# Kernel tuning notes

Hardware: AMD Instinct MI355X
Metric: run time of the kernel (lower is better)

The kernel has to match this reference:

```python
import jax, jax.numpy as jnp
import numpy as np


def setup_inputs() -> dict:
    key = jax.random.key(0)
    N, nH, D, L, P = 2, 8, 32, 4, 4
    shapes = np.array([[92, 92], [46, 46], [23, 23], [12, 12]], dtype=np.int64)
    areas = shapes[:, 0] * shapes[:, 1]
    Lin = int(areas.sum())  # 11253
    Lq = Lin  # encoder self-attention
    k1, k2, k3 = jax.random.split(key, 3)
    value = jax.random.normal(k1, (N, Lin, nH, D), dtype=jnp.float32)
    sampling_locations = jax.random.uniform(k2, (N, Lq, nH, L, P, 2), dtype=jnp.float32)
    aw = jax.random.uniform(k3, (N, Lq, nH, L, P), dtype=jnp.float32)
    attention_weights = aw / aw.sum(axis=(-2, -1), keepdims=True)  # softmax-normalized over L*P
    spatial_shapes = jnp.asarray(shapes)
    starts = np.concatenate([[0], np.cumsum(areas)[:-1]])
    level_start_index = jnp.asarray(starts, dtype=jnp.int64)
    return dict(value=value, spatial_shapes=spatial_shapes,
                level_start_index=level_start_index,
                sampling_locations=sampling_locations,
                attention_weights=attention_weights)


def _gather2d(v_nh, xi, yi, Hl, Wl):
    # v_nh: [N, nH, Hl*Wl, D]; xi, yi: [N, Lq, nH, P] int32 pixel coords
    N, Lq, nH, P = xi.shape
    valid = (xi >= 0) & (xi < Wl) & (yi >= 0) & (yi < Hl)
    xc = jnp.clip(xi, 0, Wl - 1)
    yc = jnp.clip(yi, 0, Hl - 1)
    idx = (yc * Wl + xc).transpose(0, 2, 1, 3).reshape(N, nH, Lq * P)
    vals = jax.vmap(jax.vmap(lambda v, i: v[i]))(v_nh, idx)  # [N, nH, Lq*P, D]
    vals = vals.reshape(N, nH, Lq, P, -1).transpose(0, 2, 1, 3, 4)  # [N, Lq, nH, P, D]
    return vals * valid[..., None].astype(vals.dtype)


def reference(value, spatial_shapes, level_start_index, sampling_locations, attention_weights):
    # ms_deform_attn core: per-level bilinear sampling (align_corners=False,
    # zero padding) at learned locations, weighted sum over levels and points.
    shapes_np = np.asarray(spatial_shapes)
    starts_np = np.asarray(level_start_index)
    N, Lin, nH, D = value.shape
    _, Lq, _, L, P, _ = sampling_locations.shape
    out = jnp.zeros((N, Lq, nH, D), dtype=value.dtype)
    for lvl in range(L):
        Hl, Wl = int(shapes_np[lvl, 0]), int(shapes_np[lvl, 1])
        s = int(starts_np[lvl])
        v_nh = value[:, s:s + Hl * Wl].transpose(0, 2, 1, 3)  # [N, nH, Hl*Wl, D]
        loc = sampling_locations[:, :, :, lvl]  # [N, Lq, nH, P, 2]
        # grid_sample convention: normalized [0,1] -> pixel coord, align_corners=False
        x = loc[..., 0] * Wl - 0.5
        y = loc[..., 1] * Hl - 0.5
        x0f = jnp.floor(x); y0f = jnp.floor(y)
        dx = x - x0f; dy = y - y0f
        x0 = x0f.astype(jnp.int32); y0 = y0f.astype(jnp.int32)
        x1 = x0 + 1; y1 = y0 + 1
        w00 = ((1.0 - dx) * (1.0 - dy))[..., None]
        w01 = (dx * (1.0 - dy))[..., None]
        w10 = ((1.0 - dx) * dy)[..., None]
        w11 = (dx * dy)[..., None]
        samp = (w00 * _gather2d(v_nh, x0, y0, Hl, Wl)
                + w01 * _gather2d(v_nh, x1, y0, Hl, Wl)
                + w10 * _gather2d(v_nh, x0, y1, Hl, Wl)
                + w11 * _gather2d(v_nh, x1, y1, Hl, Wl))  # [N, Lq, nH, P, D]
        aw_l = attention_weights[:, :, :, lvl]  # [N, Lq, nH, P]
        out = out + (samp * aw_l[..., None]).sum(axis=3)
    return out.reshape(N, Lq, nH * D)
```

## Files before the change

### kernel.cpp

```cpp
#include <hip/hip_runtime.h>

#define NH 8
#define DD 32
#define LL 4
#define PP 4
#define PXB (DD * 2)
#define STAGE_BYTES 43264

typedef float  f32x4  __attribute__((ext_vector_type(4)));
typedef float  f32x2  __attribute__((ext_vector_type(2)));
typedef int    i32x4  __attribute__((ext_vector_type(4)));
typedef _Float16 half4v __attribute__((ext_vector_type(4)));

__global__ __launch_bounds__(256) void conv_kernel(
    const float* __restrict__ value, _Float16* __restrict__ vh,
    int Lin, int total)
{
    int tid = blockIdx.x * blockDim.x + threadIdx.x;
    if (tid >= total) return;
    const int d4  = tid & 7;
    const int pos = (tid >> 3) % Lin;
    const int nh  = tid / (8 * Lin);
    const int n   = nh >> 3;
    const int h   = nh & 7;

    const f32x4 v = *(const f32x4*)(value + (((size_t)n * Lin + pos) * NH + h) * DD + d4 * 4);
    half4v o;
    o.x = (_Float16)v.x; o.y = (_Float16)v.y; o.z = (_Float16)v.z; o.w = (_Float16)v.w;
    *(half4v*)(vh + ((size_t)nh * Lin + pos) * DD + d4 * 4) = o;
}

#define FMAMIX_LO(ACC, DW, W) \
    asm("v_fma_mix_f32 %0, %1, %2, %0 op_sel:[0,0,0] op_sel_hi:[1,0,0]" \
        : "+v"(ACC) : "v"(DW), "v"(W))
#define FMAMIX_HI(ACC, DW, W) \
    asm("v_fma_mix_f32 %0, %1, %2, %0 op_sel:[1,0,0] op_sel_hi:[1,0,0]" \
        : "+v"(ACC) : "v"(DW), "v"(W))

__global__ __attribute__((amdgpu_flat_work_group_size(256, 256)))
void msda_fwd_h(
    const _Float16* __restrict__ vh,
    const int*   __restrict__ ssh,
    const int*   __restrict__ lsi,
    const float* __restrict__ sloc,
    const float* __restrict__ aw,
    float*       __restrict__ out,
    int N, int Lq, int Lin, int spx, int nSlabs)
{
    __shared__ i32x4 ent[32 * 41];
    __shared__ __align__(16) char stage[STAGE_BYTES];

    const int xcd   = blockIdx.x & 7;
    const int blk   = blockIdx.x >> 3;
    const int sw    = blk % spx;
    const int chunk = blk / spx;
    const int slab  = xcd * spx + sw;
    if (slab >= nSlabs) return;

    const int t  = threadIdx.x;
    const int u  = t >> 3;
    const int j  = t & 7;
    const int q  = chunk * 32 + u;
    const int qc = min(q, Lq - 1);
    const int n  = slab >> 3;
    const int h  = slab & 7;

    const bool is64 = (ssh[1] == 0);
    const int H2 = is64 ? ssh[8]  : ssh[4];
    const int W2 = is64 ? ssh[10] : ssh[5];
    const int H3 = is64 ? ssh[12] : ssh[6];
    const int W3 = is64 ? ssh[14] : ssh[7];
    const int S2 = is64 ? lsi[4]  : lsi[2];
    const int stBytes = (H2 * W2 + H3 * W3) * PXB;
    const bool staged = (stBytes <= STAGE_BYTES);

    const char* __restrict__ slabBase = (const char*)vh + (size_t)slab * Lin * PXB;

    if (staged) {
        const char* __restrict__ src = slabBase + (size_t)S2 * PXB;
        const int nch = stBytes >> 4;
        for (int i = t; i < nch; i += 256)
            *(i32x4*)(stage + (size_t)i * 16) = *(const i32x4*)(src + (size_t)i * 16);
    }

    {
        const size_t nqh = ((size_t)n * Lq + qc) * NH + h;
        const int l = j >> 1;
        const int W = is64 ? ssh[4 * l + 2] : ssh[2 * l + 1];
        const int H = is64 ? ssh[4 * l]     : ssh[2 * l];
        const int S = is64 ? lsi[2 * l]     : lsi[l];
        const f32x4 lc = __builtin_nontemporal_load((const f32x4*)sloc + nqh * 8 + j);
        const f32x2 av = __builtin_nontemporal_load((const f32x2*)aw + nqh * 8 + j);
        const float fW = (float)W, fH = (float)H;
        const int rowb  = W * PXB;
        const int sbase = (staged && l >= 2) ? (S - S2) * PXB : S * PXB;
#pragma unroll
        for (int pt = 0; pt < 2; ++pt) {
            const float x  = lc[2 * pt]     * fW - 0.5f;
            const float y  = lc[2 * pt + 1] * fH - 0.5f;
            const float wq = av[pt];
            const float x0f = floorf(x), y0f = floorf(y);
            const int x0 = (int)x0f, y0 = (int)y0f;
            const float dx = x - x0f, dy = y - y0f;
            const int x1 = x0 + 1, y1 = y0 + 1;
            const bool vx0 = (x0 >= 0) & (x0 < W), vx1 = (x1 >= 0) & (x1 < W);
            const bool vy0 = (y0 >= 0) & (y0 < H), vy1 = (y1 >= 0) & (y1 < H);
            const int cx0 = min(max(x0, 0), W - 1), cx1 = min(max(x1, 0), W - 1);
            const int cy0 = min(max(y0, 0), H - 1), cy1 = min(max(y1, 0), H - 1);
            const float wx0 = (1.f - dx) * wq * (vx0 ? 1.f : 0.f);
            const float wx1 = dx         * wq * (vx1 ? 1.f : 0.f);
            const float ty  = (1.f - dy) * (vy0 ? 1.f : 0.f);
            const float by  = dy         * (vy1 ? 1.f : 0.f);
            const int rt = cy0 * rowb + sbase;
            const int rb = cy1 * rowb + sbase;
            i32x4 e0, e1;
            e0.x = rt + cx0 * PXB;  e0.y = rb + cx0 * PXB;
            e0.z = __float_as_int(wx0 * ty);  e0.w = __float_as_int(wx0 * by);
            e1.x = rt + cx1 * PXB;  e1.y = rb + cx1 * PXB;
            e1.z = __float_as_int(wx1 * ty);  e1.w = __float_as_int(wx1 * by);
            const int base = u * 41 + 5 * j + 2 * pt;
            ent[base]     = e0;
            ent[base + 1] = e1;
        }
    }
    __syncthreads();
    if (q >= Lq) return;

    const int side = j >> 2;
    const int cg   = j & 3;
    const int cg16 = cg * 16;
    const char* __restrict__ sb = slabBase + cg16;
    const int ub = u * 41 + side;

    float acc[8];
#pragma unroll
    for (int k = 0; k < 8; ++k) acc[k] = 0.f;

#define RD(b, E) { \
    E[0] = ent[ub + 10 * (b) + 0]; \
    E[1] = ent[ub + 10 * (b) + 2]; \
    E[2] = ent[ub + 10 * (b) + 5]; \
    E[3] = ent[ub + 10 * (b) + 7]; }
#define LD(E, V) _Pragma("unroll") \
    for (int i = 0; i < 4; ++i) { \
        V[2*i]   = *(const i32x4*)(sb + (unsigned)E[i].x); \
        V[2*i+1] = *(const i32x4*)(sb + (unsigned)E[i].y); }
#define LDL(E, V) _Pragma("unroll") \
    for (int i = 0; i < 4; ++i) { \
        V[2*i]   = *(const i32x4*)(stage + (unsigned)(E[i].x + cg16)); \
        V[2*i+1] = *(const i32x4*)(stage + (unsigned)(E[i].y + cg16)); }
#define AC(E, V) _Pragma("unroll") \
    for (int i = 0; i < 4; ++i) { \
        const float wt = __int_as_float(E[i].z); \
        const float wb = __int_as_float(E[i].w); \
        _Pragma("unroll") for (int d = 0; d < 4; ++d) { \
            FMAMIX_LO(acc[2*d],   V[2*i][d],   wt); \
            FMAMIX_HI(acc[2*d+1], V[2*i][d],   wt); \
            FMAMIX_LO(acc[2*d],   V[2*i+1][d], wb); \
            FMAMIX_HI(acc[2*d+1], V[2*i+1][d], wb); } }

    i32x4 E0[4], E1[4], E2[4], E3[4];
    i32x4 V0[8], V1[8], V2[8], V3[8];
    RD(0, E0) LD(E0, V0)
    RD(1, E1) LD(E1, V1)
    RD(2, E2) RD(3, E3)
    if (staged) { LDL(E2, V2) LDL(E3, V3) }
    else        { LD(E2, V2)  LD(E3, V3)  }
    AC(E0, V0)
    AC(E1, V1)
    AC(E2, V2)
    AC(E3, V3)

#pragma unroll
    for (int k = 0; k < 8; ++k)
        acc[k] += __shfl_xor(acc[k], 4);

    f32x4 st;
    st.x = acc[side * 4 + 0];
    st.y = acc[side * 4 + 1];
    st.z = acc[side * 4 + 2];
    st.w = acc[side * 4 + 3];
    const size_t onqh = ((size_t)n * Lq + q) * NH + h;
    __builtin_nontemporal_store(st, (f32x4*)(out + onqh * DD + cg * 8 + side * 4));
}

__global__ __launch_bounds__(256) void msda_fwd_f32(
    const float* __restrict__ value,
    const int*   __restrict__ spatial_shapes,
    const int*   __restrict__ level_start,
    const float* __restrict__ sloc,
    const float* __restrict__ aw,
    float*       __restrict__ out,
    int N, int Lq, int Lin, int total)
{
    int tid = blockIdx.x * blockDim.x + threadIdx.x;
    if (tid >= total) return;
    const int c  = tid & 7;
    const int h  = (tid >> 3) & 7;
    const int nq = tid >> 6;
    const int n  = nq / Lq;
    const bool is64 = (spatial_shapes[1] == 0);
    int Hs[LL], Ws[LL], Ss[LL];
#pragma unroll
    for (int l = 0; l < LL; ++l) {
        if (is64) { Hs[l] = spatial_shapes[4*l]; Ws[l] = spatial_shapes[4*l+2]; Ss[l] = level_start[2*l]; }
        else      { Hs[l] = spatial_shapes[2*l]; Ws[l] = spatial_shapes[2*l+1]; Ss[l] = level_start[l]; }
    }
    const size_t nqh = (size_t)nq * NH + h;
    const float* loc_p = sloc + nqh * (LL * PP * 2);
    const float* aw_p  = aw   + nqh * (LL * PP);
    float4 acc = make_float4(0.f, 0.f, 0.f, 0.f);
#pragma unroll
    for (int l = 0; l < LL; ++l) {
        const int H = Hs[l], W = Ws[l];
        const float* vb = value + (((size_t)n * Lin + Ss[l]) * NH + h) * DD + c * 4;
#pragma unroll
        for (int p = 0; p < PP; ++p) {
            const int jj = l * PP + p;
            const float x = loc_p[2*jj] * (float)W - 0.5f;
            const float y = loc_p[2*jj+1] * (float)H - 0.5f;
            const float w = aw_p[jj];
            const float x0f = floorf(x), y0f = floorf(y);
            const int x0 = (int)x0f, y0 = (int)y0f, x1 = x0+1, y1 = y0+1;
            const float dx = x - x0f, dy = y - y0f;
            const bool vx0 = x0>=0 && x0<W, vx1 = x1>=0 && x1<W;
            const bool vy0 = y0>=0 && y0<H, vy1 = y1>=0 && y1<H;
            const int cx0 = min(max(x0,0),W-1), cx1 = min(max(x1,0),W-1);
            const int cy0 = min(max(y0,0),H-1), cy1 = min(max(y1,0),H-1);
            const float w00 = (1.f-dx)*(1.f-dy)*w*((vx0&&vy0)?1.f:0.f);
            const float w01 = dx*(1.f-dy)*w*((vx1&&vy0)?1.f:0.f);
            const float w10 = (1.f-dx)*dy*w*((vx0&&vy1)?1.f:0.f);
            const float w11 = dx*dy*w*((vx1&&vy1)?1.f:0.f);
            const float4 v00 = *(const float4*)(vb + (size_t)(cy0*W+cx0)*(NH*DD));
            const float4 v01 = *(const float4*)(vb + (size_t)(cy0*W+cx1)*(NH*DD));
            const float4 v10 = *(const float4*)(vb + (size_t)(cy1*W+cx0)*(NH*DD));
            const float4 v11 = *(const float4*)(vb + (size_t)(cy1*W+cx1)*(NH*DD));
            acc.x += w00*v00.x + w01*v01.x + w10*v10.x + w11*v11.x;
            acc.y += w00*v00.y + w01*v01.y + w10*v10.y + w11*v11.y;
            acc.z += w00*v00.z + w01*v01.z + w10*v10.z + w11*v11.z;
            acc.w += w00*v00.w + w01*v01.w + w10*v10.w + w11*v11.w;
        }
    }
    *(float4*)(out + nqh * DD + c * 4) = acc;
}

extern "C" void kernel_launch(void* const* d_in, const int* in_sizes, int n_in,
                              void* d_out, int out_size, void* d_ws, size_t ws_size,
                              hipStream_t stream)
{
    const float* value = (const float*)d_in[0];
    const int*   ss    = (const int*)  d_in[1];
    const int*   lsi   = (const int*)  d_in[2];
    const float* sloc  = (const float*)d_in[3];
    const float* aw    = (const float*)d_in[4];
    float* out = (float*)d_out;

    const int N = 2;
    const int Lq  = in_sizes[4] / (N * NH * LL * PP);
    const int Lin = in_sizes[0] / (N * NH * DD);

    const size_t need = (size_t)N * NH * Lin * DD * sizeof(_Float16);
    if (ws_size >= need) {
        _Float16* vh = (_Float16*)d_ws;
        const int ctotal = N * NH * Lin * 8;
        conv_kernel<<<(ctotal + 255) / 256, 256, 0, stream>>>(value, vh, Lin, ctotal);

        const int nSlabs = N * NH;
        const int spx    = (nSlabs + 7) / 8;
        const int chunks = (Lq + 31) / 32;
        const int grid   = 8 * spx * chunks;
        msda_fwd_h<<<grid, 256, 0, stream>>>(vh, ss, lsi, sloc, aw, out,
                                             N, Lq, Lin, spx, nSlabs);
    } else {
        const int total = N * Lq * NH * 8;
        msda_fwd_f32<<<(total + 255) / 256, 256, 0, stream>>>(value, ss, lsi, sloc, aw, out,
                                                              N, Lq, Lin, total);
    }
}
```

Baseline: 160.0 us.

## Stage only level-3 values in padded LDS and interleave gather loads with accumulation

Reduces the LDS staging buffer from levels 2+3 to level 3 only, with a 16-byte row pad to spread LDS bank conflicts. Level 2 is now gathered from global memory. The smaller LDS footprint plus a waves_per_eu(4) hint is meant to raise occupancy. Loads for levels 2 and 3 are reordered to interleave with accumulation of earlier levels, reducing register pressure. The conversion kernel uses nontemporal loads. The tradeoff is more global gather traffic for level 2.

After: 136.7 us. 1.17x faster.

```diff
diff --git a/kernel.cpp b/kernel.cpp
--- a/kernel.cpp
+++ b/kernel.cpp
@@ -4,8 +4,8 @@
 #define DD 32
 #define LL 4
 #define PP 4
-#define PXB (DD * 2)
-#define STAGE_BYTES 43264
+#define PXB 64
+#define STAGE_BYTES 9472
 
 typedef float  f32x4  __attribute__((ext_vector_type(4)));
 typedef float  f32x2  __attribute__((ext_vector_type(2)));
@@ -24,7 +24,8 @@
     const int n   = nh >> 3;
     const int h   = nh & 7;
 
-    const f32x4 v = *(const f32x4*)(value + (((size_t)n * Lin + pos) * NH + h) * DD + d4 * 4);
+    const f32x4 v = __builtin_nontemporal_load(
+        (const f32x4*)(value + (((size_t)n * Lin + pos) * NH + h) * DD + d4 * 4));
     half4v o;
     o.x = (_Float16)v.x; o.y = (_Float16)v.y; o.z = (_Float16)v.z; o.w = (_Float16)v.w;
     *(half4v*)(vh + ((size_t)nh * Lin + pos) * DD + d4 * 4) = o;
@@ -38,6 +39,7 @@
         : "+v"(ACC) : "v"(DW), "v"(W))
 
 __global__ __attribute__((amdgpu_flat_work_group_size(256, 256)))
+__attribute__((amdgpu_waves_per_eu(4)))
 void msda_fwd_h(
     const _Float16* __restrict__ vh,
     const int*   __restrict__ ssh,
@@ -66,21 +68,22 @@
     const int h  = slab & 7;
 
     const bool is64 = (ssh[1] == 0);
-    const int H2 = is64 ? ssh[8]  : ssh[4];
-    const int W2 = is64 ? ssh[10] : ssh[5];
     const int H3 = is64 ? ssh[12] : ssh[6];
     const int W3 = is64 ? ssh[14] : ssh[7];
-    const int S2 = is64 ? lsi[4]  : lsi[2];
-    const int stBytes = (H2 * W2 + H3 * W3) * PXB;
-    const bool staged = (stBytes <= STAGE_BYTES);
+    const int S3 = is64 ? lsi[6]  : lsi[3];
+    const int rowp = W3 * PXB + 16;
+    const bool staged = (H3 * rowp <= STAGE_BYTES);
 
     const char* __restrict__ slabBase = (const char*)vh + (size_t)slab * Lin * PXB;
 
     if (staged) {
-        const char* __restrict__ src = slabBase + (size_t)S2 * PXB;
-        const int nch = stBytes >> 4;
-        for (int i = t; i < nch; i += 256)
-            *(i32x4*)(stage + (size_t)i * 16) = *(const i32x4*)(src + (size_t)i * 16);
+        const char* __restrict__ src = slabBase + (size_t)S3 * PXB;
+        const int rowch = W3 * 4;
+        const int nch = H3 * rowch;
+        for (int i = t; i < nch; i += 256) {
+            const int r = i / rowch, c = i - r * rowch;
+            *(i32x4*)(stage + r * rowp + c * 16) = *(const i32x4*)(src + (size_t)i * 16);
+        }
     }
 
     {
@@ -92,8 +95,9 @@
         const f32x4 lc = __builtin_nontemporal_load((const f32x4*)sloc + nqh * 8 + j);
         const f32x2 av = __builtin_nontemporal_load((const f32x2*)aw + nqh * 8 + j);
         const float fW = (float)W, fH = (float)H;
-        const int rowb  = W * PXB;
-        const int sbase = (staged && l >= 2) ? (S - S2) * PXB : S * PXB;
+        const bool st3 = staged && (l == 3);
+        const int rowb  = st3 ? rowp : W * PXB;
+        const int sbase = st3 ? 0    : S * PXB;
 #pragma unroll
         for (int pt = 0; pt < 2; ++pt) {
             const float x  = lc[2 * pt]     * fW - 0.5f;
@@ -163,11 +167,12 @@
     i32x4 V0[8], V1[8], V2[8], V3[8];
     RD(0, E0) LD(E0, V0)
     RD(1, E1) LD(E1, V1)
-    RD(2, E2) RD(3, E3)
-    if (staged) { LDL(E2, V2) LDL(E3, V3) }
-    else        { LD(E2, V2)  LD(E3, V3)  }
     AC(E0, V0)
+    RD(2, E2) LD(E2, V2)
     AC(E1, V1)
+    RD(3, E3)
+    if (staged) { LDL(E3, V3) }
+    else        { LD(E3, V3)  }
     AC(E2, V2)
     AC(E3, V3)
 
```
